# Kernel optimization log

Hardware: AMD Instinct MI355X
Metric: run time of the kernel (lower is better)

## Reference

```python
import jax, jax.numpy as jnp
import numpy as np

T, B, OBS, H, ACT = 256, 1024, 256, 256, 64
SLOPE = 0.1


def setup_inputs() -> dict:
    key = jax.random.key(0)
    ks = jax.random.split(key, 20)
    stdv = 1.0 / np.sqrt(H)
    u = lambda k, shape: jax.random.uniform(k, shape, jnp.float32, -stdv, stdv)
    return {
        "x": jax.random.normal(ks[0], (T, B, OBS), jnp.float32),
        "noise1": jax.random.uniform(ks[1], (T, B, 1), jnp.float32),
        "noise2": jax.random.uniform(ks[2], (T, B, 1), jnp.float32),
        # FCEncoder: two Linear+ReLU layers
        "We1": u(ks[3], (OBS, H)), "be1": u(ks[4], (H,)),
        "We2": u(ks[5], (H, H)), "be2": u(ks[6], (H,)),
        # cell_1 (bottom): U_11 [bottom,4H+1], U_21 [top,4H+1], W_01 [H,4H+1], bias
        "U11_1": u(ks[7], (H, 4 * H + 1)), "U21_1": u(ks[8], (H, 4 * H + 1)),
        "W01_1": u(ks[9], (H, 4 * H + 1)), "b1": u(ks[10], (4 * H + 1,)),
        # cell_2 (top, last layer): no U_21
        "U11_2": u(ks[11], (H, 4 * H + 1)), "W01_2": u(ks[12], (H, 4 * H + 1)),
        "b2": u(ks[13], (4 * H + 1,)),
        "Wh": u(ks[14], (H, H)), "bh": u(ks[15], (H,)),
        "Wp": u(ks[16], (H, ACT)), "bp": u(ks[17], (ACT,)),
    }


def _trigger_train(z_hat, noise):
    # forward: (noise < z_hat).float(); backward: 0.1 * identity (straight-through)
    hard = (noise < z_hat).astype(z_hat.dtype)
    return jax.lax.stop_gradient(hard) + 0.1 * (z_hat - jax.lax.stop_gradient(z_hat))


def _gates(f_s):
    f = jax.nn.sigmoid(f_s[:, 0:H])
    i = jax.nn.sigmoid(f_s[:, H:2 * H])
    o = jax.nn.sigmoid(f_s[:, 2 * H:3 * H])
    g = jnp.tanh(f_s[:, 3 * H:4 * H])
    z_hat = jnp.clip((SLOPE * f_s[:, 4 * H:4 * H + 1] + 1.0) / 2.0, 0.05, 0.95)
    return f, i, o, g, z_hat


def reference(x, noise1, noise2, We1, be1, We2, be2,
              U11_1, U21_1, W01_1, b1, U11_2, W01_2, b2, Wh, bh, Wp, bp):
    # encoder over all timesteps at once (parallel_wrapper equivalent)
    xe = jax.nn.relu(jnp.einsum('tbi,ih->tbh', x, We1) + be1)
    xe = jax.nn.relu(jnp.einsum('tbi,ih->tbh', xe, We2) + be2)

    def step(carry, inp):
        h1, c1, z1, h2, c2 = carry
        xt, n1, n2 = inp
        # ---- cell 1 (not last layer; z_bottom = 1) ----
        fs1 = h1 @ W01_1 + z1 * (h2 @ U21_1) + xt @ U11_1 + b1
        f, i, o, g, zhat1 = _gates(fs1)
        c1n = f * c1 + i * g              # z_bottom == 1 everywhere
        h1n = o * jnp.tanh(c1n)
        z1n = _trigger_train(zhat1, n1)
        # ---- cell 2 (last layer; z_bottom = z1n, s_topdown = 0) ----
        fs2 = h2 @ W01_2 + z1n * (h1n @ U11_2) + b2
        f2, i2, o2, g2, zhat2 = _gates(fs2)
        c2n = (1.0 - z1n) * c2 + z1n * (f2 * c2 + i2 * g2)
        h2n = o2 * jnp.tanh(c2n)
        _ = _trigger_train(zhat2, n2)
        return (h1n, c1n, z1n, h2n, c2n), h2n

    zeros = jnp.zeros((B, H), jnp.float32)
    init = (zeros, zeros, jnp.ones((B, 1), jnp.float32), zeros, zeros)
    _, emb = jax.lax.scan(step, init, (xe, noise1, noise2))  # emb: [T,B,H]

    hid = jax.nn.relu(jnp.einsum('tbh,hk->tbk', emb, Wh) + bh)
    pred = jnp.tanh(jnp.einsum('tbh,ha->tba', hid, Wp) + bp)
    return pred
```

## Files before the change

kernel.cpp:

```cpp
#include <hip/hip_runtime.h>
#include <math.h>

typedef __attribute__((ext_vector_type(8))) _Float16 half8;
typedef __attribute__((ext_vector_type(4))) _Float16 half4;
typedef __attribute__((ext_vector_type(4))) float    f32x4;
typedef unsigned long long u64;

#define NSTEP 256
#define CH    32
#define NCHUNK (NSTEP/CH)
#define NB    1024
#define HID   256
#define BH    262144
#define LK    40
#define EXS   20
#define INV2K 4.8828125e-4f
#define SEQ_SMEM 98304

__device__ __forceinline__ float sigf(float x){ return 1.f/(1.f+expf(-x)); }
__device__ __forceinline__ void splitf(float v, _Float16& h, _Float16& l){
    h = (_Float16)v; l = (_Float16)((v - (float)h)*2048.f);
}
union H4U { half4 v; u64 u; };

__global__ __launch_bounds__(256)
void wsplit_k(const float* __restrict__ s0, const float* __restrict__ s1,
              const float* __restrict__ s2, int K, int N, int ldn,
              int kb1, int kb2, _Float16* __restrict__ oh, _Float16* __restrict__ ol)
{
    int idx = blockIdx.x*256 + threadIdx.x;
    if (idx >= N*K) return;
    int n = idx / K, k = idx - n*K;
    const float* s = (k < kb1) ? &s0[(size_t)k*ldn]
                   : (k < kb2) ? &s1[(size_t)(k-kb1)*ldn]
                               : &s2[(size_t)(k-kb2)*ldn];
    float v = s[n];
    _Float16 h, l; splitf(v, h, l);
    oh[idx] = h; ol[idx] = l;
}

__global__ void wz_k(const float* __restrict__ W01, const float* __restrict__ U21,
                     const float* __restrict__ U11, float* __restrict__ wz)
{
    int k = blockIdx.x*256 + threadIdx.x;
    if (k >= 768) return;
    wz[k] = (k < 256) ? W01[(size_t)k*1025 + 1024]
          : (k < 512) ? U21[(size_t)(k-256)*1025 + 1024]
                      : U11[(size_t)(k-512)*1025 + 1024];
}

__global__ __launch_bounds__(256)
void init_k(_Float16* h1H, _Float16* h1L, _Float16* h2H, _Float16* h2L,
            float* c1g, float* c2g, unsigned* zr)
{
    int i = blockIdx.x*256 + threadIdx.x;
    h1H[i] = (_Float16)0.f; h1L[i] = (_Float16)0.f;
    h2H[i] = (_Float16)0.f; h2L[i] = (_Float16)0.f;
    c1g[i] = 0.f; c2g[i] = 0.f;
    if (i < NB) zr[i] = 1u;
}

template<int AIN, int AOUT, int NCOL>
__global__ __launch_bounds__(256)
void gemm_t(const float* __restrict__ Af,
            const _Float16* __restrict__ Ah_, const _Float16* __restrict__ Al_,
            const _Float16* __restrict__ Bh_, const _Float16* __restrict__ Bl_,
            const float* __restrict__ bias,
            _Float16* __restrict__ Oh, _Float16* __restrict__ Ol,
            float* __restrict__ Of)
{
    constexpr int NT = 8;
    __shared__ __align__(16) char smem[40960];

    const int tid  = threadIdx.x;
    const size_t R0 = (size_t)blockIdx.x*64;
    const int C0   = blockIdx.y*64;
    const int rh   = (tid>>6)&1, ch = tid>>7;
    const int lane = tid&63, lr = lane&15, kq = (lane>>4)<<3;
    const int arow = tid>>2, seg = tid&3;
    const size_t abase = (R0+arow)*256 + seg*8;
    const size_t wbase = (size_t)(C0 + (tid>>2))*256 + seg*8;

    f32x4 am[2][2], ax[2][2];
#pragma unroll
    for (int r=0;r<2;++r)
#pragma unroll
        for (int c=0;c<2;++c){ am[r][c]=(f32x4)0.f; ax[r][c]=(f32x4)0.f; }

    half8 rah, ral, rwh, rwl;
    auto load_tile = [&](int k0, half8& ah, half8& al, half8& wh, half8& wl) {
        if (AIN == 0) {
            float4 a0 = *(const float4*)(Af + abase + k0);
            float4 a1 = *(const float4*)(Af + abase + k0 + 4);
            float av[8] = {a0.x,a0.y,a0.z,a0.w,a1.x,a1.y,a1.z,a1.w};
#pragma unroll
            for (int i=0;i<8;++i){ _Float16 h,l; splitf(av[i],h,l); ah[i]=h; al[i]=l; }
        } else {
            ah = *(const half8*)(Ah_ + abase + k0);
            al = *(const half8*)(Al_ + abase + k0);
        }
        wh = *(const half8*)(Bh_ + wbase + k0);
        wl = *(const half8*)(Bl_ + wbase + k0);
    };
    auto store_tile = [&](int buf) {
        char* bs = smem + buf*20480;
        *(half8*)((_Float16*)(bs        ) + arow*LK + seg*8) = rah;
        *(half8*)((_Float16*)(bs +  5120) + arow*LK + seg*8) = ral;
        *(half8*)((_Float16*)(bs + 10240) + (tid>>2)*LK + seg*8) = rwh;
        *(half8*)((_Float16*)(bs + 15360) + (tid>>2)*LK + seg*8) = rwl;
    };

    load_tile(0, rah, ral, rwh, rwl);
    store_tile(0);

#pragma unroll 2
    for (int kb = 0; kb < NT; ++kb) {
        const int buf = kb & 1;
        half8 nah, nal, nwh, nwl;
        if (kb+1 < NT) load_tile((kb+1)*32, nah, nal, nwh, nwl);
        __syncthreads();
        const char* bs = smem + buf*20480;
        const _Float16* LAh = (const _Float16*)bs;
        const _Float16* LAl = (const _Float16*)(bs +  5120);
        const _Float16* LBh = (const _Float16*)(bs + 10240);
        const _Float16* LBl = (const _Float16*)(bs + 15360);
        half8 fah[2], fal[2], fbh[2], fbl[2];
#pragma unroll
        for (int rf=0;rf<2;++rf) {
            fah[rf] = *(const half8*)(LAh + (rh*32+rf*16+lr)*LK + kq);
            fal[rf] = *(const half8*)(LAl + (rh*32+rf*16+lr)*LK + kq);
        }
#pragma unroll
        for (int cf=0;cf<2;++cf) {
            fbh[cf] = *(const half8*)(LBh + (ch*32+cf*16+lr)*LK + kq);
            fbl[cf] = *(const half8*)(LBl + (ch*32+cf*16+lr)*LK + kq);
        }
#pragma unroll
        for (int cf=0;cf<2;++cf)
#pragma unroll
            for (int rf=0;rf<2;++rf) {
                am[rf][cf] = __builtin_amdgcn_mfma_f32_16x16x32_f16(fah[rf], fbh[cf], am[rf][cf],0,0,0);
                ax[rf][cf] = __builtin_amdgcn_mfma_f32_16x16x32_f16(fah[rf], fbl[cf], ax[rf][cf],0,0,0);
                ax[rf][cf] = __builtin_amdgcn_mfma_f32_16x16x32_f16(fal[rf], fbh[cf], ax[rf][cf],0,0,0);
            }
        if (kb+1 < NT) {
            rah=nah; ral=nal; rwh=nwh; rwl=nwl;
            store_tile((kb+1)&1);
        }
    }

#pragma unroll
    for (int cf=0;cf<2;++cf) {
        int col = C0 + ch*32 + cf*16 + lr;
        float bcol = bias[col];
#pragma unroll
        for (int rf=0;rf<2;++rf)
#pragma unroll
            for (int q=0;q<4;++q) {
                size_t row = R0 + rh*32 + rf*16 + ((lane>>4)<<2) + q;
                float v = am[rf][cf][q] + ax[rf][cf][q]*INV2K + bcol;
                if (AOUT == 0) {
                    v = fmaxf(v, 0.f);
                    _Float16 h,l; splitf(v,h,l);
                    Oh[row*NCOL + col] = h;
                    Ol[row*NCOL + col] = l;
                } else {
                    Of[row*NCOL + col] = tanhf(v);
                }
            }
    }
}

struct PArgs {
    const _Float16 *XeH, *XeL;
    _Float16 *EmH, *EmL;
    const _Float16 *W1h, *W1l, *W2h, *W2l;
    const float *b1, *b2, *wz, *noise;
    _Float16 *h1rH, *h1rL, *h2rH, *h2rL;
    unsigned *zr;
    float *c1g, *c2g;
    unsigned *ctr;
    unsigned *tick;
    int chunk;
};

__device__ __forceinline__ void xbarrier(unsigned* c, int tid)
{
    __syncthreads();
    if (tid == 0) {
        __hip_atomic_fetch_add(c, 1u, __ATOMIC_RELAXED, __HIP_MEMORY_SCOPE_AGENT);
        int guard = 0;
        while (__hip_atomic_load(c, __ATOMIC_RELAXED, __HIP_MEMORY_SCOPE_AGENT) < 16u
               && guard < (1<<19)) {
            __builtin_amdgcn_s_sleep(2);
            ++guard;
        }
    }
    __syncthreads();
}

__global__ __launch_bounds__(512, 1)
void hm_pers_k(PArgs a)
{
    extern __shared__ __align__(16) char smem[];
    float* ex = (float*)smem;

    const int tid = threadIdx.x, wv = tid>>6, lane = tid&63;

    unsigned* pan_sh = (unsigned*)(smem + 61440);
    if (tid == 0) {
        unsigned xcc;
        asm volatile("s_getreg_b32 %0, hwreg(HW_REG_XCC_ID)" : "=s"(xcc));
        xcc &= 7u;
        unsigned slot = __hip_atomic_fetch_add(a.tick + a.chunk*8 + xcc, 1u,
                          __ATOMIC_RELAXED, __HIP_MEMORY_SCOPE_AGENT);
        pan_sh[0] = (xcc + 8u*(slot>>4)) & 15u;
        pan_sh[1] = slot & 15u;
    }
    __syncthreads();
    const int panel = pan_sh[0], cs = pan_sh[1];

    const int g  = wv>>1, rh = wv&1;
    const int lr = lane&15, kq = (lane>>4)<<3;
    const int R0 = panel*64, j0 = cs*16;
    const int srow = tid>>3, skq = (tid&7)*4;
    const int gcol = (srow>>4)*256 + j0 + (srow&15);
    const size_t w1base = (size_t)gcol*768 + skq;
    const size_t w2base = (size_t)gcol*512 + skq;
    const size_t arbase = (size_t)(R0+srow)*HID;
    const float bv1 = a.b1[g*256 + j0 + lr];
    const float bv2 = a.b2[g*256 + j0 + lr];
    const bool do_z = (cs == 0);

    const int urow = (tid & 255)>>2, ujj = (tid&3)*4;
    const size_t ubase = (size_t)(R0+urow)*HID + j0 + ujj;

    float c1s[4], c2s[4];
    if (tid < 256) {
        float4 cv1 = *(const float4*)(a.c1g + ubase);
        float4 cv2 = *(const float4*)(a.c2g + ubase);
        c1s[0]=cv1.x; c1s[1]=cv1.y; c1s[2]=cv1.z; c1s[3]=cv1.w;
        c2s[0]=cv2.x; c2s[1]=cv2.y; c2s[2]=cv2.z; c2s[3]=cv2.w;
    }

#pragma unroll 1
    for (int s = 0; s < CH; ++s) {
        const int t = a.chunk*CH + s;
        const _Float16* h1cH = a.h1rH + (size_t)s*BH;
        const _Float16* h1cL = a.h1rL + (size_t)s*BH;
        _Float16*       h1nH = a.h1rH + (size_t)(s+1)*BH;
        _Float16*       h1nL = a.h1rL + (size_t)(s+1)*BH;
        const _Float16* h2cH = a.h2rH + (size_t)s*BH;
        const _Float16* h2cL = a.h2rL + (size_t)s*BH;
        _Float16*       h2nH = a.h2rH + (size_t)(s+1)*BH;
        _Float16*       h2nL = a.h2rL + (size_t)(s+1)*BH;
        const unsigned* zc = a.zr + (size_t)s*NB;
        unsigned*       zn = a.zr + (size_t)(s+1)*NB;
        const _Float16* xeh = a.XeH + (size_t)t*BH;
        const _Float16* xel = a.XeL + (size_t)t*BH;

        const unsigned zrv = zc[R0+srow];
        f32x4 am[2], ax[2];
        am[0]=(f32x4)0.f; am[1]=(f32x4)0.f; ax[0]=(f32x4)0.f; ax[1]=(f32x4)0.f;
        float zacc = 0.f;
        u64 Ah_[2], Al_[2], Wh_[2], Wl_[2];

        auto p1_load = [&](int kt, int sl){
            int kg = kt*32 + skq;
            u64 hv, lv;
            if (kg < 256)      { hv = *(const u64*)(h1cH + arbase + kg);
                                 lv = *(const u64*)(h1cL + arbase + kg); }
            else if (kg < 512) {
                if (zrv) { hv = *(const u64*)(h2cH + arbase + (kg-256));
                           lv = *(const u64*)(h2cL + arbase + (kg-256)); }
                else     { hv = 0; lv = 0; }
            } else             { hv = *(const u64*)(xeh + arbase + (kg-512));
                                 lv = *(const u64*)(xel + arbase + (kg-512)); }
            Ah_[sl]=hv; Al_[sl]=lv;
            Wh_[sl] = *(const u64*)(a.W1h + w1base + (size_t)kt*32);
            Wl_[sl] = *(const u64*)(a.W1l + w1base + (size_t)kt*32);
        };
        auto p2_load = [&](int kt, int sl, unsigned zg){
            int kg = kt*32 + skq;
            u64 hv, lv;
            if (kg < 256)      { hv = *(const u64*)(h2cH + arbase + kg);
                                 lv = *(const u64*)(h2cL + arbase + kg); }
            else {
                if (zg) { hv = *(const u64*)(h1nH + arbase + (kg-256));
                          lv = *(const u64*)(h1nL + arbase + (kg-256)); }
                else    { hv = 0; lv = 0; }
            }
            Ah_[sl]=hv; Al_[sl]=lv;
            Wh_[sl] = *(const u64*)(a.W2h + w2base + (size_t)kt*32);
            Wl_[sl] = *(const u64*)(a.W2l + w2base + (size_t)kt*32);
        };
        auto stg = [&](int buf, int sl){
            char* bs = smem + buf*20480;
            *(u64*)((_Float16*)(bs        ) + srow*LK + skq) = Ah_[sl];
            *(u64*)((_Float16*)(bs +  5120) + srow*LK + skq) = Al_[sl];
            *(u64*)((_Float16*)(bs + 10240) + srow*LK + skq) = Wh_[sl];
            *(u64*)((_Float16*)(bs + 15360) + srow*LK + skq) = Wl_[sl];
        };
        auto cmp = [&](int buf, int kt, bool dz){
            const char* bs = smem + buf*20480;
            const _Float16* LAh = (const _Float16*)bs;
            const _Float16* LAl = (const _Float16*)(bs +  5120);
            const _Float16* LBh = (const _Float16*)(bs + 10240);
            const _Float16* LBl = (const _Float16*)(bs + 15360);
            half8 fbh = *(const half8*)(LBh + (g*16+lr)*LK + kq);
            half8 fbl = *(const half8*)(LBl + (g*16+lr)*LK + kq);
#pragma unroll
            for (int rf=0; rf<2; ++rf) {
                half8 fah = *(const half8*)(LAh + (rh*32+rf*16+lr)*LK + kq);
                half8 fal = *(const half8*)(LAl + (rh*32+rf*16+lr)*LK + kq);
                am[rf] = __builtin_amdgcn_mfma_f32_16x16x32_f16(fah, fbh, am[rf],0,0,0);
                ax[rf] = __builtin_amdgcn_mfma_f32_16x16x32_f16(fah, fbl, ax[rf],0,0,0);
                ax[rf] = __builtin_amdgcn_mfma_f32_16x16x32_f16(fal, fbh, ax[rf],0,0,0);
            }
            if (dz) {
#pragma unroll
                for (int i=0;i<4;++i) {
                    float av = (float)LAh[srow*LK + skq + i]
                             + (float)LAl[srow*LK + skq + i]*INV2K;
                    zacc = fmaf(av, a.wz[kt*32 + skq + i], zacc);
                }
            }
        };

        p1_load(0,0); p1_load(1,1);
        stg(0,0);
#pragma unroll
        for (int kt = 0; kt < 24; ++kt) {
            if (kt+2 < 24) p1_load(kt+2, kt&1);
            __syncthreads();
            cmp(kt%3, kt, do_z);
            if (kt+1 < 24) stg((kt+1)%3, (kt+1)&1);
        }
        __syncthreads();

#pragma unroll
        for (int rf=0; rf<2; ++rf)
#pragma unroll
            for (int q=0;q<4;++q) {
                float v = am[rf][q] + ax[rf][q]*INV2K + bv1;
                v = (g<3) ? sigf(v) : tanhf(v);
                int row = rh*32 + rf*16 + ((lane>>4)<<2) + q;
                ex[(g*64+row)*EXS + lr] = v;
            }
        if (do_z) {
            float sum = zacc;
            sum += __shfl_xor(sum, 1);
            sum += __shfl_xor(sum, 2);
            sum += __shfl_xor(sum, 4);
            if ((tid&7) == 0) {
                float fsz = sum + a.b1[1024];
                float zh = fminf(fmaxf((0.1f*fsz + 1.f)*0.5f, 0.05f), 0.95f);
                unsigned zv = (a.noise[(size_t)t*NB + R0+srow] < zh) ? 1u : 0u;
                zn[R0+srow] = zv;
                if (s == CH-1) a.zr[R0+srow] = zv;
            }
        }
        __syncthreads();
        if (tid < 256) {
            half4 hh, hl;
#pragma unroll
            for (int q=0;q<4;++q) {
                float f0 = ex[(0*64+urow)*EXS + ujj + q];
                float i0 = ex[(1*64+urow)*EXS + ujj + q];
                float o0 = ex[(2*64+urow)*EXS + ujj + q];
                float g0 = ex[(3*64+urow)*EXS + ujj + q];
                float cn = f0*c1s[q] + i0*g0;
                c1s[q] = cn;
                float hv = o0*tanhf(cn);
                _Float16 h,l; splitf(hv,h,l); hh[q]=h; hl[q]=l;
            }
            H4U ph_, pl_; ph_.v = hh; pl_.v = hl;
            *(u64*)(h1nH + ubase) = ph_.u;
            *(u64*)(h1nL + ubase) = pl_.u;
            if (s == CH-1) {
                *(u64*)(a.h1rH + ubase) = ph_.u;
                *(u64*)(a.h1rL + ubase) = pl_.u;
            }
        }
        xbarrier(a.ctr + ((size_t)(a.chunk*CH + s)*2 + 0)*16 + panel, tid);

        const unsigned zrv2 = zn[R0+srow];
        am[0]=(f32x4)0.f; am[1]=(f32x4)0.f; ax[0]=(f32x4)0.f; ax[1]=(f32x4)0.f;

        p2_load(0,0,zrv2); p2_load(1,1,zrv2);
        stg(0,0);
#pragma unroll
        for (int kt = 0; kt < 16; ++kt) {
            if (kt+2 < 16) p2_load(kt+2, kt&1, zrv2);
            __syncthreads();
            cmp(kt%3, kt, false);
            if (kt+1 < 16) stg((kt+1)%3, (kt+1)&1);
        }
        __syncthreads();

#pragma unroll
        for (int rf=0; rf<2; ++rf)
#pragma unroll
            for (int q=0;q<4;++q) {
                float v = am[rf][q] + ax[rf][q]*INV2K + bv2;
                v = (g<3) ? sigf(v) : tanhf(v);
                int row = rh*32 + rf*16 + ((lane>>4)<<2) + q;
                ex[(g*64+row)*EXS + lr] = v;
            }
        __syncthreads();
        if (tid < 256) {
            unsigned zun = zn[R0+urow];
            half4 hh, hl;
#pragma unroll
            for (int q=0;q<4;++q) {
                float f0 = ex[(0*64+urow)*EXS + ujj + q];
                float i0 = ex[(1*64+urow)*EXS + ujj + q];
                float o0 = ex[(2*64+urow)*EXS + ujj + q];
                float g0 = ex[(3*64+urow)*EXS + ujj + q];
                float cn = zun ? (f0*c2s[q] + i0*g0) : c2s[q];
                c2s[q] = cn;
                float hv = o0*tanhf(cn);
                _Float16 h,l; splitf(hv,h,l); hh[q]=h; hl[q]=l;
            }
            H4U ph_, pl_; ph_.v = hh; pl_.v = hl;
            *(u64*)(h2nH + ubase) = ph_.u;
            *(u64*)(h2nL + ubase) = pl_.u;
            *(u64*)(a.EmH + (size_t)t*BH + ubase) = ph_.u;
            *(u64*)(a.EmL + (size_t)t*BH + ubase) = pl_.u;
            if (s == CH-1) {
                *(u64*)(a.h2rH + ubase) = ph_.u;
                *(u64*)(a.h2rL + ubase) = pl_.u;
            }
        }
        xbarrier(a.ctr + ((size_t)(a.chunk*CH + s)*2 + 1)*16 + panel, tid);
    }

    if (tid < 256) {
        *(float4*)(a.c1g + ubase) = float4{c1s[0],c1s[1],c1s[2],c1s[3]};
        *(float4*)(a.c2g + ubase) = float4{c2s[0],c2s[1],c2s[2],c2s[3]};
    }
}

extern "C" void kernel_launch(void* const* d_in, const int* in_sizes, int n_in,
                              void* d_out, int out_size, void* d_ws, size_t ws_size,
                              hipStream_t stream)
{
    const float* x     = (const float*)d_in[0];
    const float* n1    = (const float*)d_in[1];
    const float* We1   = (const float*)d_in[3];
    const float* be1   = (const float*)d_in[4];
    const float* We2   = (const float*)d_in[5];
    const float* be2   = (const float*)d_in[6];
    const float* U11_1 = (const float*)d_in[7];
    const float* U21_1 = (const float*)d_in[8];
    const float* W01_1 = (const float*)d_in[9];
    const float* b1    = (const float*)d_in[10];
    const float* U11_2 = (const float*)d_in[11];
    const float* W01_2 = (const float*)d_in[12];
    const float* b2    = (const float*)d_in[13];
    const float* Wh    = (const float*)d_in[14];
    const float* bh    = (const float*)d_in[15];
    const float* Wp    = (const float*)d_in[16];
    const float* bp_   = (const float*)d_in[17];
    float* out = (float*)d_out;

    char* p = (char*)d_ws;
    auto alloc = [&](size_t bytes){ char* q = p; p += (bytes + 255) & ~(size_t)255; return q; };
    _Float16* XeH  = (_Float16*)alloc((size_t)NSTEP*BH*2);
    _Float16* XeL  = (_Float16*)alloc((size_t)NSTEP*BH*2);
    _Float16* EmH  = (_Float16*)alloc((size_t)NSTEP*BH*2);
    _Float16* EmL  = (_Float16*)alloc((size_t)NSTEP*BH*2);
    _Float16* Wt1h = (_Float16*)alloc((size_t)1024*768*2);
    _Float16* Wt1l = (_Float16*)alloc((size_t)1024*768*2);
    _Float16* Wt2h = (_Float16*)alloc((size_t)1024*512*2);
    _Float16* Wt2l = (_Float16*)alloc((size_t)1024*512*2);
    _Float16* We1h = (_Float16*)alloc(256*256*2);
    _Float16* We1l = (_Float16*)alloc(256*256*2);
    _Float16* We2h = (_Float16*)alloc(256*256*2);
    _Float16* We2l = (_Float16*)alloc(256*256*2);
    _Float16* Whh  = (_Float16*)alloc(256*256*2);
    _Float16* Whl  = (_Float16*)alloc(256*256*2);
    _Float16* Wph  = (_Float16*)alloc(64*256*2);
    _Float16* Wpl  = (_Float16*)alloc(64*256*2);
    float*    wz1  = (float*)alloc(768*4);
    _Float16* h1rH = (_Float16*)alloc((size_t)(CH+1)*BH*2);
    _Float16* h1rL = (_Float16*)alloc((size_t)(CH+1)*BH*2);
    _Float16* h2rH = (_Float16*)alloc((size_t)(CH+1)*BH*2);
    _Float16* h2rL = (_Float16*)alloc((size_t)(CH+1)*BH*2);
    unsigned* zr   = (unsigned*)alloc((size_t)(CH+1)*NB*4);
    float*    c1g  = (float*)alloc((size_t)BH*4);
    float*    c2g  = (float*)alloc((size_t)BH*4);
    unsigned* ctr  = (unsigned*)alloc((size_t)NCHUNK*CH*2*16*4);
    unsigned* tick = (unsigned*)alloc((size_t)NCHUNK*8*4);
    if (ws_size < (size_t)(p - (char*)d_ws)) return;

    _Float16* TmpH = EmH; _Float16* TmpL = EmL;
    _Float16* TpH  = XeH; _Float16* TpL  = XeL;

    wsplit_k<<<dim3(3072), 256, 0, stream>>>(W01_1, U21_1, U11_1, 768, 1024, 1025, 256, 512, Wt1h, Wt1l);
    wsplit_k<<<dim3(2048), 256, 0, stream>>>(W01_2, U11_2, nullptr, 512, 1024, 1025, 256, 512, Wt2h, Wt2l);
    wsplit_k<<<dim3(256),  256, 0, stream>>>(We1, nullptr, nullptr, 256, 256, 256, 256, 256, We1h, We1l);
    wsplit_k<<<dim3(256),  256, 0, stream>>>(We2, nullptr, nullptr, 256, 256, 256, 256, 256, We2h, We2l);
    wsplit_k<<<dim3(256),  256, 0, stream>>>(Wh,  nullptr, nullptr, 256, 256, 256, 256, 256, Whh,  Whl);
    wsplit_k<<<dim3(64),   256, 0, stream>>>(Wp,  nullptr, nullptr, 256, 64, 64, 256, 256, Wph, Wpl);
    wz_k<<<dim3(3), 256, 0, stream>>>(W01_1, U21_1, U11_1, wz1);
    init_k<<<dim3(1024), 256, 0, stream>>>(h1rH, h1rL, h2rH, h2rL, c1g, c2g, zr);
    hipMemsetAsync(ctr, 0, (size_t)NCHUNK*CH*2*16*4, stream);
    hipMemsetAsync(tick, 0, (size_t)NCHUNK*8*4, stream);

    for (int c = 0; c < 8; ++c) {
        size_t ro = (size_t)c*32*BH;
        gemm_t<0,0,256><<<dim3(512,4), 256, 0, stream>>>(
            x + ro, nullptr, nullptr, We1h, We1l, be1, TmpH, TmpL, nullptr);
        gemm_t<1,0,256><<<dim3(512,4), 256, 0, stream>>>(
            nullptr, TmpH, TmpL, We2h, We2l, be2, XeH + ro, XeL + ro, nullptr);
    }

    hipFuncSetAttribute((const void*)hm_pers_k, hipFuncAttributeMaxDynamicSharedMemorySize, SEQ_SMEM);
    PArgs pa;
    pa.XeH = XeH; pa.XeL = XeL; pa.EmH = EmH; pa.EmL = EmL;
    pa.W1h = Wt1h; pa.W1l = Wt1l; pa.W2h = Wt2h; pa.W2l = Wt2l;
    pa.b1 = b1; pa.b2 = b2; pa.wz = wz1; pa.noise = n1;
    pa.h1rH = h1rH; pa.h1rL = h1rL; pa.h2rH = h2rH; pa.h2rL = h2rL;
    pa.zr = zr; pa.c1g = c1g; pa.c2g = c2g; pa.ctr = ctr; pa.tick = tick;
    for (int c = 0; c < NCHUNK; ++c) {
        pa.chunk = c;
        void* kargs[] = { (void*)&pa };
        hipLaunchCooperativeKernel((const void*)hm_pers_k, dim3(256), dim3(512),
                                   kargs, SEQ_SMEM, stream);
    }

    for (int c = 0; c < 8; ++c) {
        size_t ro = (size_t)c*32*BH;
        gemm_t<1,0,256><<<dim3(512,4), 256, 0, stream>>>(
            nullptr, EmH + ro, EmL + ro, Whh, Whl, bh, TpH, TpL, nullptr);
        gemm_t<1,1,64><<<dim3(512,1), 256, 0, stream>>>(
            nullptr, TpH, TpL, Wph, Wpl, bp_, nullptr, nullptr,
            out + (size_t)c*32*NB*64);
    }
}
```

Baseline: 8.056 ms.

## Keep cell-1 weight slice resident in LDS and retile persistent recurrence kernel

```diff
diff --git a/kernel.cpp b/kernel.cpp
--- a/kernel.cpp
+++ b/kernel.cpp
@@ -2,7 +2,6 @@
 #include <math.h>
 
 typedef __attribute__((ext_vector_type(8))) _Float16 half8;
-typedef __attribute__((ext_vector_type(4))) _Float16 half4;
 typedef __attribute__((ext_vector_type(4))) float    f32x4;
 typedef unsigned long long u64;
 
@@ -13,15 +12,22 @@
 #define HID   256
 #define BH    262144
 #define LK    40
-#define EXS   20
+#define LK1   776
 #define INV2K 4.8828125e-4f
-#define SEQ_SMEM 98304
+
+#define W1H_OFF 0
+#define W1L_OFF 49664
+#define AB_OFF  99328
+#define W2_OFF  140288
+#define PAN_OFF 150528
+#define SEQ_SMEM 150784
+#define EX_OFF  AB_OFF
 
 __device__ __forceinline__ float sigf(float x){ return 1.f/(1.f+expf(-x)); }
 __device__ __forceinline__ void splitf(float v, _Float16& h, _Float16& l){
     h = (_Float16)v; l = (_Float16)((v - (float)h)*2048.f);
 }
-union H4U { half4 v; u64 u; };
+union H2U { _Float16 h[2]; unsigned u; };
 
 __global__ __launch_bounds__(256)
 void wsplit_k(const float* __restrict__ s0, const float* __restrict__ s1,
@@ -190,8 +196,8 @@
     if (tid == 0) {
         __hip_atomic_fetch_add(c, 1u, __ATOMIC_RELAXED, __HIP_MEMORY_SCOPE_AGENT);
         int guard = 0;
-        while (__hip_atomic_load(c, __ATOMIC_RELAXED, __HIP_MEMORY_SCOPE_AGENT) < 16u
-               && guard < (1<<19)) {
+        while (__hip_atomic_load(c, __ATOMIC_RELAXED, __HIP_MEMORY_SCOPE_AGENT) < 32u
+               && guard < (1<<16)) {
             __builtin_amdgcn_s_sleep(2);
             ++guard;
         }
@@ -203,45 +209,67 @@
 void hm_pers_k(PArgs a)
 {
     extern __shared__ __align__(16) char smem[];
-    float* ex = (float*)smem;
 
     const int tid = threadIdx.x, wv = tid>>6, lane = tid&63;
 
-    unsigned* pan_sh = (unsigned*)(smem + 61440);
+    unsigned* pan_sh = (unsigned*)(smem + PAN_OFF);
     if (tid == 0) {
         unsigned xcc;
         asm volatile("s_getreg_b32 %0, hwreg(HW_REG_XCC_ID)" : "=s"(xcc));
         xcc &= 7u;
         unsigned slot = __hip_atomic_fetch_add(a.tick + a.chunk*8 + xcc, 1u,
                           __ATOMIC_RELAXED, __HIP_MEMORY_SCOPE_AGENT);
-        pan_sh[0] = (xcc + 8u*(slot>>4)) & 15u;
-        pan_sh[1] = slot & 15u;
+        pan_sh[0] = xcc;
+        pan_sh[1] = slot & 31u;
     }
     __syncthreads();
     const int panel = pan_sh[0], cs = pan_sh[1];
 
-    const int g  = wv>>1, rh = wv&1;
-    const int lr = lane&15, kq = (lane>>4)<<3;
-    const int R0 = panel*64, j0 = cs*16;
-    const int srow = tid>>3, skq = (tid&7)*4;
-    const int gcol = (srow>>4)*256 + j0 + (srow&15);
-    const size_t w1base = (size_t)gcol*768 + skq;
-    const size_t w2base = (size_t)gcol*512 + skq;
-    const size_t arbase = (size_t)(R0+srow)*HID;
-    const float bv1 = a.b1[g*256 + j0 + lr];
-    const float bv2 = a.b2[g*256 + j0 + lr];
+    const int rg = wv & 3, cg = wv >> 2;
+    const int lr = lane & 15, kq = (lane>>4) << 3;
+    const int R0 = panel * 128;
+    const int j0h = cs * 8;
+    const int srow = tid >> 2, seg = tid & 3;
+    const size_t arbase = (size_t)(R0 + srow) * HID;
     const bool do_z = (cs == 0);
 
-    const int urow = (tid & 255)>>2, ujj = (tid&3)*4;
-    const size_t ubase = (size_t)(R0+urow)*HID + j0 + ujj;
-
-    float c1s[4], c2s[4];
-    if (tid < 256) {
-        float4 cv1 = *(const float4*)(a.c1g + ubase);
-        float4 cv2 = *(const float4*)(a.c2g + ubase);
-        c1s[0]=cv1.x; c1s[1]=cv1.y; c1s[2]=cv1.z; c1s[3]=cv1.w;
-        c2s[0]=cv2.x; c2s[1]=cv2.y; c2s[2]=cv2.z; c2s[3]=cv2.w;
-    }
+    const int fcl  = cg*16 + lr;
+    const int gate = fcl >> 3;
+    const int jc   = fcl & 7;
+    const float bv1 = a.b1[gate*256 + j0h + jc];
+    const float bv2 = a.b2[gate*256 + j0h + jc];
+
+    const int hl2 = (tid >= 128) & 1;
+    const int tt2 = tid & 127;
+    const int fc2 = tt2 >> 2, sg2 = tt2 & 3;
+    const _Float16* W2src = hl2 ? a.W2l : a.W2h;
+    const size_t w2base = (size_t)((fc2>>3)*256 + j0h + (fc2&7))*512 + sg2*8;
+
+#pragma unroll
+    for (int it = 0; it < 12; ++it) {
+        int idx = it*512 + tid;
+        int hl  = idx >= 3072;
+        int e   = idx - hl*3072;
+        int fc  = e / 96;
+        int ks  = e - fc*96;
+        const _Float16* src = (hl ? a.W1l : a.W1h)
+            + (size_t)((fc>>3)*256 + j0h + (fc&7))*768 + ks*8;
+        *(half8*)(smem + (hl ? W1L_OFF : W1H_OFF) + (fc*LK1 + ks*8)*2)
+            = *(const half8*)src;
+    }
+    __syncthreads();
+
+    const int urow = tid >> 2, ujj = (tid & 3)*2;
+    const size_t ubase = (size_t)(R0 + urow)*HID + j0h + ujj;
+
+    float c1s[2], c2s[2];
+    {
+        float2 cv1 = *(const float2*)(a.c1g + ubase);
+        float2 cv2 = *(const float2*)(a.c2g + ubase);
+        c1s[0]=cv1.x; c1s[1]=cv1.y; c2s[0]=cv2.x; c2s[1]=cv2.y;
+    }
+
+    float* ex = (float*)(smem + EX_OFF);
 
 #pragma unroll 1
     for (int s = 0; s < CH; ++s) {
@@ -263,78 +291,58 @@
         f32x4 am[2], ax[2];
         am[0]=(f32x4)0.f; am[1]=(f32x4)0.f; ax[0]=(f32x4)0.f; ax[1]=(f32x4)0.f;
         float zacc = 0.f;
-        u64 Ah_[2], Al_[2], Wh_[2], Wl_[2];
+        half8 rAh[2], rAl[2], rW[2];
 
         auto p1_load = [&](int kt, int sl){
-            int kg = kt*32 + skq;
-            u64 hv, lv;
-            if (kg < 256)      { hv = *(const u64*)(h1cH + arbase + kg);
-                                 lv = *(const u64*)(h1cL + arbase + kg); }
+            int kg = kt*32 + seg*8;
+            half8 hv, lv;
+            if (kg < 256)      { hv = *(const half8*)(h1cH + arbase + kg);
+                                 lv = *(const half8*)(h1cL + arbase + kg); }
             else if (kg < 512) {
-                if (zrv) { hv = *(const u64*)(h2cH + arbase + (kg-256));
-                           lv = *(const u64*)(h2cL + arbase + (kg-256)); }
-                else     { hv = 0; lv = 0; }
-            } else             { hv = *(const u64*)(xeh + arbase + (kg-512));
-                                 lv = *(const u64*)(xel + arbase + (kg-512)); }
-            Ah_[sl]=hv; Al_[sl]=lv;
-            Wh_[sl] = *(const u64*)(a.W1h + w1base + (size_t)kt*32);
-            Wl_[sl] = *(const u64*)(a.W1l + w1base + (size_t)kt*32);
+                if (zrv) { hv = *(const half8*)(h2cH + arbase + (kg-256));
+                           lv = *(const half8*)(h2cL + arbase + (kg-256)); }
+                else     { hv = half8{}; lv = half8{}; }
+            } else             { hv = *(const half8*)(xeh + arbase + (kg-512));
+                                 lv = *(const half8*)(xel + arbase + (kg-512)); }
+            rAh[sl]=hv; rAl[sl]=lv;
         };
-        auto p2_load = [&](int kt, int sl, unsigned zg){
-            int kg = kt*32 + skq;
-            u64 hv, lv;
-            if (kg < 256)      { hv = *(const u64*)(h2cH + arbase + kg);
-                                 lv = *(const u64*)(h2cL + arbase + kg); }
-            else {
-                if (zg) { hv = *(const u64*)(h1nH + arbase + (kg-256));
-                          lv = *(const u64*)(h1nL + arbase + (kg-256)); }
-                else    { hv = 0; lv = 0; }
-            }
-            Ah_[sl]=hv; Al_[sl]=lv;
-            Wh_[sl] = *(const u64*)(a.W2h + w2base + (size_t)kt*32);
-            Wl_[sl] = *(const u64*)(a.W2l + w2base + (size_t)kt*32);
+        auto stgA = [&](int buf, int sl){
+            *(half8*)(smem + AB_OFF + buf*20480         + (srow*LK + seg*8)*2) = rAh[sl];
+            *(half8*)(smem + AB_OFF + buf*20480 + 10240 + (srow*LK + seg*8)*2) = rAl[sl];
         };
-        auto stg = [&](int buf, int sl){
-            char* bs = smem + buf*20480;
-            *(u64*)((_Float16*)(bs        ) + srow*LK + skq) = Ah_[sl];
-            *(u64*)((_Float16*)(bs +  5120) + srow*LK + skq) = Al_[sl];
-            *(u64*)((_Float16*)(bs + 10240) + srow*LK + skq) = Wh_[sl];
-            *(u64*)((_Float16*)(bs + 15360) + srow*LK + skq) = Wl_[sl];
-        };
-        auto cmp = [&](int buf, int kt, bool dz){
-            const char* bs = smem + buf*20480;
-            const _Float16* LAh = (const _Float16*)bs;
-            const _Float16* LAl = (const _Float16*)(bs +  5120);
-            const _Float16* LBh = (const _Float16*)(bs + 10240);
-            const _Float16* LBl = (const _Float16*)(bs + 15360);
-            half8 fbh = *(const half8*)(LBh + (g*16+lr)*LK + kq);
-            half8 fbl = *(const half8*)(LBl + (g*16+lr)*LK + kq);
+        auto cmp1 = [&](int buf, int kt){
+            const _Float16* LAh = (const _Float16*)(smem + AB_OFF + buf*20480);
+            const _Float16* LAl = (const _Float16*)(smem + AB_OFF + buf*20480 + 10240);
+            const int bo = fcl*LK1 + kt*32 + kq;
+            half8 fbh = *(const half8*)((const _Float16*)(smem + W1H_OFF) + bo);
+            half8 fbl = *(const half8*)((const _Float16*)(smem + W1L_OFF) + bo);
 #pragma unroll
             for (int rf=0; rf<2; ++rf) {
-                half8 fah = *(const half8*)(LAh + (rh*32+rf*16+lr)*LK + kq);
-                half8 fal = *(const half8*)(LAl + (rh*32+rf*16+lr)*LK + kq);
+                const int ao = (rg*32 + rf*16 + lr)*LK + kq;
+                half8 fah = *(const half8*)(LAh + ao);
+                half8 fal = *(const half8*)(LAl + ao);
                 am[rf] = __builtin_amdgcn_mfma_f32_16x16x32_f16(fah, fbh, am[rf],0,0,0);
                 ax[rf] = __builtin_amdgcn_mfma_f32_16x16x32_f16(fah, fbl, ax[rf],0,0,0);
                 ax[rf] = __builtin_amdgcn_mfma_f32_16x16x32_f16(fal, fbh, ax[rf],0,0,0);
             }
-            if (dz) {
-#pragma unroll
-                for (int i=0;i<4;++i) {
-                    float av = (float)LAh[srow*LK + skq + i]
-                             + (float)LAl[srow*LK + skq + i]*INV2K;
-                    zacc = fmaf(av, a.wz[kt*32 + skq + i], zacc);
+            if (do_z) {
+#pragma unroll
+                for (int i=0;i<8;++i) {
+                    float av = (float)LAh[srow*LK + seg*8 + i]
+                             + (float)LAl[srow*LK + seg*8 + i]*INV2K;
+                    zacc = fmaf(av, a.wz[kt*32 + seg*8 + i], zacc);
                 }
             }
         };
 
         p1_load(0,0); p1_load(1,1);
-        stg(0,0);
+        stgA(0,0);
 #pragma unroll
         for (int kt = 0; kt < 24; ++kt) {
             if (kt+2 < 24) p1_load(kt+2, kt&1);
             __syncthreads();
-            cmp(kt%3, kt, do_z);
-            if (kt+1 < 24) stg((kt+1)%3, (kt+1)&1);
+            cmp1(kt&1, kt);
+            if (kt+1 < 24) stgA((kt+1)&1, (kt+1)&1);
         }
         __syncthreads();
 
@@ -343,16 +351,15 @@
 #pragma unroll
             for (int q=0;q<4;++q) {
                 float v = am[rf][q] + ax[rf][q]*INV2K + bv1;
-                v = (g<3) ? sigf(v) : tanhf(v);
-                int row = rh*32 + rf*16 + ((lane>>4)<<2) + q;
-                ex[(g*64+row)*EXS + lr] = v;
+                v = (gate<3) ? sigf(v) : tanhf(v);
+                int row = rg*32 + rf*16 + ((lane>>4)<<2) + q;
+                ex[(gate*128 + row)*9 + jc] = v;
             }
         if (do_z) {
             float sum = zacc;
             sum += __shfl_xor(sum, 1);
             sum += __shfl_xor(sum, 2);
-            sum += __shfl_xor(sum, 4);
-            if ((tid&7) == 0) {
+            if (seg == 0) {
                 float fsz = sum + a.b1[1024];
                 float zh = fminf(fmaxf((0.1f*fsz + 1.f)*0.5f, 0.05f), 0.95f);
                 unsigned zv = (a.noise[(size_t)t*NB + R0+srow] < zh) ? 1u : 0u;
@@ -361,40 +368,75 @@
             }
         }
         __syncthreads();
-        if (tid < 256) {
-            half4 hh, hl;
-#pragma unroll
-            for (int q=0;q<4;++q) {
-                float f0 = ex[(0*64+urow)*EXS + ujj + q];
-                float i0 = ex[(1*64+urow)*EXS + ujj + q];
-                float o0 = ex[(2*64+urow)*EXS + ujj + q];
-                float g0 = ex[(3*64+urow)*EXS + ujj + q];
+        {
+            H2U hh, hl;
+#pragma unroll
+            for (int q=0;q<2;++q) {
+                float f0 = ex[(0*128+urow)*9 + ujj + q];
+                float i0 = ex[(1*128+urow)*9 + ujj + q];
+                float o0 = ex[(2*128+urow)*9 + ujj + q];
+                float g0 = ex[(3*128+urow)*9 + ujj + q];
                 float cn = f0*c1s[q] + i0*g0;
                 c1s[q] = cn;
                 float hv = o0*tanhf(cn);
-                _Float16 h,l; splitf(hv,h,l); hh[q]=h; hl[q]=l;
-            }
-            H4U ph_, pl_; ph_.v = hh; pl_.v = hl;
-            *(u64*)(h1nH + ubase) = ph_.u;
-            *(u64*)(h1nL + ubase) = pl_.u;
+                _Float16 h,l; splitf(hv,h,l); hh.h[q]=h; hl.h[q]=l;
+            }
+            *(unsigned*)(h1nH + ubase) = hh.u;
+            *(unsigned*)(h1nL + ubase) = hl.u;
             if (s == CH-1) {
-                *(u64*)(a.h1rH + ubase) = ph_.u;
-                *(u64*)(a.h1rL + ubase) = pl_.u;
-            }
-        }
-        xbarrier(a.ctr + ((size_t)(a.chunk*CH + s)*2 + 0)*16 + panel, tid);
+                *(unsigned*)(a.h1rH + ubase) = hh.u;
+                *(unsigned*)(a.h1rL + ubase) = hl.u;
+            }
+        }
+        xbarrier(a.ctr + ((size_t)(a.chunk*CH + s)*2 + 0)*8 + panel, tid);
 
         const unsigned zrv2 = zn[R0+srow];
         am[0]=(f32x4)0.f; am[1]=(f32x4)0.f; ax[0]=(f32x4)0.f; ax[1]=(f32x4)0.f;
 
-        p2_load(0,0,zrv2); p2_load(1,1,zrv2);
-        stg(0,0);
+        auto p2_load = [&](int kt, int sl){
+            int kg = kt*32 + seg*8;
+            half8 hv, lv;
+            if (kg < 256)      { hv = *(const half8*)(h2cH + arbase + kg);
+                                 lv = *(const half8*)(h2cL + arbase + kg); }
+            else {
+                if (zrv2) { hv = *(const half8*)(h1nH + arbase + (kg-256));
+                            lv = *(const half8*)(h1nL + arbase + (kg-256)); }
+                else      { hv = half8{}; lv = half8{}; }
+            }
+            rAh[sl]=hv; rAl[sl]=lv;
+            if (tid < 256) rW[sl] = *(const half8*)(W2src + w2base + kt*32);
+        };
+        auto stg2 = [&](int buf, int sl){
+            *(half8*)(smem + AB_OFF + buf*20480         + (srow*LK + seg*8)*2) = rAh[sl];
+            *(half8*)(smem + AB_OFF + buf*20480 + 10240 + (srow*LK + seg*8)*2) = rAl[sl];
+            if (tid < 256)
+                *(half8*)(smem + W2_OFF + buf*5120 + hl2*2560 + (fc2*LK + sg2*8)*2) = rW[sl];
+        };
+        auto cmp2 = [&](int buf){
+            const _Float16* LAh = (const _Float16*)(smem + AB_OFF + buf*20480);
+            const _Float16* LAl = (const _Float16*)(smem + AB_OFF + buf*20480 + 10240);
+            const int bo = fcl*LK + kq;
+            half8 fbh = *(const half8*)((const _Float16*)(smem + W2_OFF + buf*5120) + bo);
+            half8 fbl = *(const half8*)((const _Float16*)(smem + W2_OFF + buf*5120 + 2560) + bo);
+#pragma unroll
+            for (int rf=0; rf<2; ++rf) {
+                const int ao = (rg*32 + rf*16 + lr)*LK + kq;
+                half8 fah = *(const half8*)(LAh + ao);
+                half8 fal = *(const half8*)(LAl + ao);
+                am[rf] = __builtin_amdgcn_mfma_f32_16x16x32_f16(fah, fbh, am[rf],0,0,0);
+                ax[rf] = __builtin_amdgcn_mfma_f32_16x16x32_f16(fah, fbl, ax[rf],0,0,0);
+                ax[rf] = __builtin_amdgcn_mfma_f32_16x16x32_f16(fal, fbh, ax[rf],0,0,0);
+            }
+        };
+
+        p2_load(0,0); p2_load(1,1);
+        stg2(0,0);
 #pragma unroll
         for (int kt = 0; kt < 16; ++kt) {
-            if (kt+2 < 16) p2_load(kt+2, kt&1, zrv2);
+            if (kt+2 < 16) p2_load(kt+2, kt&1);
             __syncthreads();
-            cmp(kt%3, kt, false);
-            if (kt+1 < 16) stg((kt+1)%3, (kt+1)&1);
+            cmp2(kt&1);
+            if (kt+1 < 16) stg2((kt+1)&1, (kt+1)&1);
         }
         __syncthreads();
 
@@ -403,42 +445,39 @@
 #pragma unroll
             for (int q=0;q<4;++q) {
                 float v = am[rf][q] + ax[rf][q]*INV2K + bv2;
-                v = (g<3) ? sigf(v) : tanhf(v);
-                int row = rh*32 + rf*16 + ((lane>>4)<<2) + q;
-                ex[(g*64+row)*EXS + lr] = v;
+                v = (gate<3) ? sigf(v) : tanhf(v);
+                int row = rg*32 + rf*16 + ((lane>>4)<<2) + q;
+                ex[(gate*128 + row)*9 + jc] = v;
             }
         __syncthreads();
-        if (tid < 256) {
+        {
             unsigned zun = zn[R0+urow];
-            half4 hh, hl;
-#pragma unroll
-            for (int q=0;q<4;++q) {
-                float f0 = ex[(0*64+urow)*EXS + ujj + q];
-                float i0 = ex[(1*64+urow)*EXS + ujj + q];
-                float o0 = ex[(2*64+urow)*EXS + ujj + q];
-                float g0 = ex[(3*64+urow)*EXS + ujj + q];
+            H2U hh, hl;
+#pragma unroll
+            for (int q=0;q<2;++q) {
+                float f0 = ex[(0*128+urow)*9 + ujj + q];
+                float i0 = ex[(1*128+urow)*9 + ujj + q];
+                float o0 = ex[(2*128+urow)*9 + ujj + q];
+                float g0 = ex[(3*128+urow)*9 + ujj + q];
                 float cn = zun ? (f0*c2s[q] + i0*g0) : c2s[q];
                 c2s[q] = cn;
                 float hv = o0*tanhf(cn);
-                _Float16 h,l; splitf(hv,h,l); hh[q]=h; hl[q]=l;
-            }
-            H4U ph_, pl_; ph_.v = hh; pl_.v = hl;
-            *(u64*)(h2nH + ubase) = ph_.u;
-            *(u64*)(h2nL + ubase) = pl_.u;
-            *(u64*)(a.EmH + (size_t)t*BH + ubase) = ph_.u;
-            *(u64*)(a.EmL + (size_t)t*BH + ubase) = pl_.u;
+                _Float16 h,l; splitf(hv,h,l); hh.h[q]=h; hl.h[q]=l;
+            }
+            *(unsigned*)(h2nH + ubase) = hh.u;
+            *(unsigned*)(h2nL + ubase) = hl.u;
+            *(unsigned*)(a.EmH + (size_t)t*BH + ubase) = hh.u;
+            *(unsigned*)(a.EmL + (size_t)t*BH + ubase) = hl.u;
             if (s == CH-1) {
-                *(u64*)(a.h2rH + ubase) = ph_.u;
-                *(u64*)(a.h2rL + ubase) = pl_.u;
-            }
-        }
-        xbarrier(a.ctr + ((size_t)(a.chunk*CH + s)*2 + 1)*16 + panel, tid);
-    }
-
-    if (tid < 256) {
-        *(float4*)(a.c1g + ubase) = float4{c1s[0],c1s[1],c1s[2],c1s[3]};
-        *(float4*)(a.c2g + ubase) = float4{c2s[0],c2s[1],c2s[2],c2s[3]};
-    }
+                *(unsigned*)(a.h2rH + ubase) = hh.u;
+                *(unsigned*)(a.h2rL + ubase) = hl.u;
+            }
+        }
+        xbarrier(a.ctr + ((size_t)(a.chunk*CH + s)*2 + 1)*8 + panel, tid);
+    }
+
+    *(float2*)(a.c1g + ubase) = float2{c1s[0], c1s[1]};
+    *(float2*)(a.c2g + ubase) = float2{c2s[0], c2s[1]};
 }
 
 extern "C" void kernel_launch(void* const* d_in, const int* in_sizes, int n_in,
@@ -490,7 +529,7 @@
     unsigned* zr   = (unsigned*)alloc((size_t)(CH+1)*NB*4);
     float*    c1g  = (float*)alloc((size_t)BH*4);
     float*    c2g  = (float*)alloc((size_t)BH*4);
-    unsigned* ctr  = (unsigned*)alloc((size_t)NCHUNK*CH*2*16*4);
+    unsigned* ctr  = (unsigned*)alloc((size_t)NCHUNK*CH*2*8*4);
     unsigned* tick = (unsigned*)alloc((size_t)NCHUNK*8*4);
     if (ws_size < (size_t)(p - (char*)d_ws)) return;
 
@@ -505,8 +544,8 @@
     wsplit_k<<<dim3(64),   256, 0, stream>>>(Wp,  nullptr, nullptr, 256, 64, 64, 256, 256, Wph, Wpl);
     wz_k<<<dim3(3), 256, 0, stream>>>(W01_1, U21_1, U11_1, wz1);
     init_k<<<dim3(1024), 256, 0, stream>>>(h1rH, h1rL, h2rH, h2rL, c1g, c2g, zr);
-    hipMemsetAsync(ctr, 0, (size_t)NCHUNK*CH*2*16*4, stream);
-    hipMemsetAsync(tick, 0, (size_t)NCHUNK*8*4, stream);
+    (void)hipMemsetAsync(ctr, 0, (size_t)NCHUNK*CH*2*8*4, stream);
+    (void)hipMemsetAsync(tick, 0, (size_t)NCHUNK*8*4, stream);
 
     for (int c = 0; c < 8; ++c) {
         size_t ro = (size_t)c*32*BH;
@@ -516,7 +555,8 @@
             nullptr, TmpH, TmpL, We2h, We2l, be2, XeH + ro, XeL + ro, nullptr);
     }
 
-    hipFuncSetAttribute((const void*)hm_pers_k, hipFuncAttributeMaxDynamicSharedMemorySize, SEQ_SMEM);
+    (void)hipFuncSetAttribute((const void*)hm_pers_k,
+        hipFuncAttributeMaxDynamicSharedMemorySize, SEQ_SMEM);
     PArgs pa;
     pa.XeH = XeH; pa.XeL = XeL; pa.EmH = EmH; pa.EmL = EmL;
     pa.W1h = Wt1h; pa.W1l = Wt1l; pa.W2h = Wt2h; pa.W2l = Wt2l;
@@ -526,8 +566,8 @@
     for (int c = 0; c < NCHUNK; ++c) {
         pa.chunk = c;
         void* kargs[] = { (void*)&pa };
-        hipLaunchCooperativeKernel((const void*)hm_pers_k, dim3(256), dim3(512),
-                                   kargs, SEQ_SMEM, stream);
+        (void)hipLaunchCooperativeKernel((const void*)hm_pers_k, dim3(256), dim3(512),
+                                         kargs, SEQ_SMEM, stream);
     }
 
     for (int c = 0; c < 8; ++c) {
```

Result: faster. 7.312 ms (-9.2%).
